# Optimization experiments

Hardware: AMD Instinct MI355X
Metric: run time of the kernel (lower is better)

## Reference

```python
import jax, jax.numpy as jnp
import numpy as np
import math

HEAD_DIM = 64
N_NEWTON_ITER = 6


def _top_k_sum_selection(T, select_number, mask):
    # T: [B,H,N,D]; mask: [B,N] int (True/1 => masked out for selection, per source)
    B, H, N, D = T.shape
    big = jnp.finfo(T.dtype).max
    # select_type == 'sum' -> non-absolute row sums over feature dim, excluding token 0
    somme = jnp.sum(T[:, :, 1:, :], axis=-1)                      # [B,H,N-1]
    somme = jnp.where(mask[:, None, 1:].astype(bool), -big, somme)
    top = jax.lax.top_k(somme, select_number - 1)[1] + 1          # [B,H,M-1]
    top = jnp.concatenate(
        [top, jnp.zeros((B, H, 1), dtype=top.dtype)], axis=-1)    # always keep token 0
    index = jnp.sort(top, axis=-1)                                 # [B,H,M]
    nt = jnp.take_along_axis(T, index[..., None], axis=2)          # [B,H,M,D]
    return nt, index


def _m_matrix_composition(C, r_index):
    # C: [B,H,N,M]; r_index: [B,H,M] -> gather selected rows -> [B,H,M,M]
    return jnp.take_along_axis(C, r_index[..., None], axis=2)


def _iterative_inv(mat, n_iter=N_NEWTON_ITER):
    M = mat.shape[-1]
    I = jnp.eye(M, dtype=mat.dtype)
    Km = mat
    # init_option == 'original': global max of column sums
    V = (1.0 / jnp.max(jnp.sum(Km, axis=-2))) * jnp.swapaxes(Km, -1, -2)
    for _ in range(n_iter):
        KV = jnp.matmul(Km, V)
        V = jnp.matmul(0.25 * V,
                       13.0 * I - jnp.matmul(KV, 15.0 * I - jnp.matmul(KV, 7.0 * I - KV)))
    return V


def setup_inputs() -> dict:
    key = jax.random.key(0)
    k1, k2, k3, k4 = jax.random.split(key, 4)
    B, H, N, D = 4, 8, 4096, 64
    return {
        "Q": jax.random.normal(k1, (B, H, N, D), dtype=jnp.float32),
        "K": jax.random.normal(k2, (B, H, N, D), dtype=jnp.float32),
        "V": jax.random.normal(k3, (B, H, N, D), dtype=jnp.float32),
        "mask": jax.random.randint(k4, (B, N), 0, 2, dtype=jnp.int32),
        "select_number": 64,
    }


def reference(Q, K, V, mask, select_number):
    big = jnp.finfo(Q.dtype).max
    Qs = Q / math.sqrt(HEAD_DIM)
    nc, _ = _top_k_sum_selection(K, select_number, mask)           # [B,H,M,D]
    nr, r_index = _top_k_sum_selection(Qs, select_number, mask)    # [B,H,M,D]
    c = jnp.einsum('bhnd,bhmd->bhnm', Qs, nc)                      # [B,H,N,M]
    r = jnp.einsum('bhmd,bhnd->bhmn', nr, K)                       # [B,H,M,N]
    # forward path fills where ~mask (mask==0 => masked)
    r = jnp.where(mask[:, None, None, :].astype(bool), r, -big)
    kernel_1 = jax.nn.softmax(c, axis=-1)                          # [B,H,N,M]
    u = _m_matrix_composition(kernel_1, r_index)                   # [B,H,M,M]
    kernel_3 = jax.nn.softmax(r, axis=-1)                          # [B,H,M,N]
    kernel_2_inv = _iterative_inv(u)                               # [B,H,M,M]
    X = jnp.matmul(kernel_1, jnp.matmul(kernel_2_inv, jnp.matmul(kernel_3, V)))
    return X
```

## Files before the change

### kernel.cpp

```cpp
#include <hip/hip_runtime.h>
#include <float.h>

#define BB 4
#define HH 8
#define BHN 32
#define NTOK 4096
#define DD 64
#define MM 64
#define PAD 68
#define GPART 16

typedef _Float16 f16;
typedef __attribute__((ext_vector_type(4))) _Float16 f16x4;
typedef __attribute__((ext_vector_type(8))) _Float16 f16x8;
typedef __attribute__((ext_vector_type(4))) float f32x4;

union V8U { f16x8 v; f16x4 q[2]; };

__device__ __forceinline__ void fsplit(float v, f16* h, f16* l) {
  f16 hh = (f16)v;
  *h = hh;
  *l = (f16)(v - (float)hh);
}

__device__ __forceinline__ f32x4 mm2(f16x8 a0, f16x8 a1, f16x8 b0, f16x8 b1) {
  f32x4 c = {0.f, 0.f, 0.f, 0.f};
  c = __builtin_amdgcn_mfma_f32_16x16x32_f16(a0, b0, c, 0, 0, 0);
  c = __builtin_amdgcn_mfma_f32_16x16x32_f16(a1, b1, c, 0, 0, 0);
  return c;
}

__device__ __forceinline__ f32x4 mm6(f16x8 ah0, f16x8 ah1, f16x8 al0, f16x8 al1,
                                     f16x8 bh0, f16x8 bh1, f16x8 bl0, f16x8 bl1) {
  f32x4 a = {0.f, 0.f, 0.f, 0.f};
  f32x4 b = {0.f, 0.f, 0.f, 0.f};
  a = __builtin_amdgcn_mfma_f32_16x16x32_f16(ah0, bh0, a, 0, 0, 0);
  a = __builtin_amdgcn_mfma_f32_16x16x32_f16(ah0, bl0, a, 0, 0, 0);
  a = __builtin_amdgcn_mfma_f32_16x16x32_f16(al0, bh0, a, 0, 0, 0);
  b = __builtin_amdgcn_mfma_f32_16x16x32_f16(ah1, bh1, b, 0, 0, 0);
  b = __builtin_amdgcn_mfma_f32_16x16x32_f16(ah1, bl1, b, 0, 0, 0);
  b = __builtin_amdgcn_mfma_f32_16x16x32_f16(al1, bh1, b, 0, 0, 0);
  return a + b;
}

template<int LDA, int LDB>
__device__ __forceinline__ void mm_acc(float acc[4][4],
    const float (*A)[LDA], const float (*B)[LDB], int ti, int tj) {
  #pragma unroll
  for (int k4 = 0; k4 < 16; ++k4) {
    float a[4][4], b[4][4];
    #pragma unroll
    for (int x = 0; x < 4; ++x) {
      float4 t = *(const float4*)&A[ti*4+x][k4*4];
      a[x][0]=t.x; a[x][1]=t.y; a[x][2]=t.z; a[x][3]=t.w;
    }
    #pragma unroll
    for (int kk = 0; kk < 4; ++kk) {
      float4 t = *(const float4*)&B[k4*4+kk][tj*4];
      b[kk][0]=t.x; b[kk][1]=t.y; b[kk][2]=t.z; b[kk][3]=t.w;
    }
    #pragma unroll
    for (int kk = 0; kk < 4; ++kk)
      #pragma unroll
      for (int x = 0; x < 4; ++x)
        #pragma unroll
        for (int y = 0; y < 4; ++y)
          acc[x][y] = fmaf(a[x][kk], b[kk][y], acc[x][y]);
  }
}

__global__ __launch_bounds__(256) void k_somme(const float* __restrict__ Kg,
    const float* __restrict__ Qg, const int* __restrict__ mask,
    float* __restrict__ somK, float* __restrict__ somQ) {
  int tid = threadIdx.x;
  int lane = tid & 63;
  long grow = (long)blockIdx.x * 16 + (tid >> 6) * 4 + (lane >> 4);
  int which = grow >= (long)(BHN * NTOK);
  long row = which ? grow - (long)BHN * NTOK : grow;
  int n = (int)(row & (NTOK - 1));
  int bh = (int)(row >> 12);
  int b = bh >> 3;
  const float* src = which ? Qg : Kg;
  float4 v = *((const float4*)(src + row * DD) + (lane & 15));
  float s = v.x + v.y + v.z + v.w;
  s += __shfl_xor(s, 1); s += __shfl_xor(s, 2);
  s += __shfl_xor(s, 4); s += __shfl_xor(s, 8);
  if ((lane & 15) == 0) {
    float out = (n == 0 || mask[b * NTOK + n] != 0) ? -FLT_MAX : s;
    (which ? somQ : somK)[row] = out;
  }
}

__global__ __launch_bounds__(256) void k_select(const float* __restrict__ Kg,
    const float* __restrict__ Qg, const float* __restrict__ somK,
    const float* __restrict__ somQ, float* __restrict__ nc, float* __restrict__ nr) {
  int bh = blockIdx.x;
  int which = blockIdx.y;
  __shared__ unsigned int keys[NTOK];
  __shared__ unsigned int wb[4][256];
  __shared__ int wsum[4];
  __shared__ int wsumB[4];
  __shared__ int sh_bin, sh_need;
  __shared__ int sel[MM];
  int tid = threadIdx.x, wave = tid >> 6, lane = tid & 63;
  const float* som = (which ? somQ : somK) + (long)bh * NTOK;
  for (int i = tid; i < NTOK; i += 256) {
    float f = som[i];
    unsigned int u = __float_as_uint(f);
    u = (u & 0x80000000u) ? ~u : (u | 0x80000000u);
    keys[i] = (i == 0) ? 0u : u;
  }
  unsigned int pref = 0; int need = MM - 1;
  for (int pass = 0; pass < 4; ++pass) {
    int shift = 24 - pass * 8;
    unsigned int pm = (pass == 0) ? 0u : (0xFFFFFFFFu << (32 - 8 * pass));
    unsigned int* wbf = (unsigned int*)wb;
    wbf[tid] = 0; wbf[tid + 256] = 0; wbf[tid + 512] = 0; wbf[tid + 768] = 0;
    __syncthreads();
    for (int i = tid; i < NTOK; i += 256) {
      unsigned int k = keys[i];
      if ((k & pm) == pref) atomicAdd(&wb[wave][(k >> shift) & 255], 1u);
    }
    __syncthreads();
    int binr = 255 - tid;
    int cnt = (int)(wb[0][binr] + wb[1][binr] + wb[2][binr] + wb[3][binr]);
    int v = cnt;
    #pragma unroll
    for (int d = 1; d < 64; d <<= 1) {
      int t = __shfl_up(v, d);
      if (lane >= d) v += t;
    }
    if (lane == 63) wsum[wave] = v;
    __syncthreads();
    int off = 0;
    #pragma unroll
    for (int w = 0; w < 4; ++w) off += (w < wave) ? wsum[w] : 0;
    v += off;
    int above = v - cnt;
    if (v >= need && above < need) { sh_bin = binr; sh_need = need - above; }
    __syncthreads();
    pref |= ((unsigned int)sh_bin) << shift;
    need = sh_need;
  }
  unsigned int thr = pref;

  int base = tid * 16;
  int ctie = 0;
  #pragma unroll
  for (int j = 0; j < 16; ++j) ctie += (keys[base + j] == thr);
  int v2 = ctie;
  #pragma unroll
  for (int d = 1; d < 64; d <<= 1) {
    int t = __shfl_up(v2, d);
    if (lane >= d) v2 += t;
  }
  if (lane == 63) wsum[wave] = v2;
  __syncthreads();
  int offt = 0;
  #pragma unroll
  for (int w = 0; w < 4; ++w) offt += (w < wave) ? wsum[w] : 0;
  int tie_excl = v2 + offt - ctie;

  int tieoff = tie_excl, cnt2 = 0;
  #pragma unroll
  for (int j = 0; j < 16; ++j) {
    unsigned int k = keys[base + j];
    int f = (k > thr) ? 1 : 0;
    if (k == thr) { f = (tieoff < need) ? 1 : 0; ++tieoff; }
    if (base + j == 0) f = 1;
    cnt2 += f;
  }
  int v3 = cnt2;
  #pragma unroll
  for (int d = 1; d < 64; d <<= 1) {
    int t = __shfl_up(v3, d);
    if (lane >= d) v3 += t;
  }
  if (lane == 63) wsumB[wave] = v3;
  __syncthreads();
  int offc = 0;
  #pragma unroll
  for (int w = 0; w < 4; ++w) offc += (w < wave) ? wsumB[w] : 0;
  int o = v3 + offc - cnt2;
  tieoff = tie_excl;
  #pragma unroll
  for (int j = 0; j < 16; ++j) {
    unsigned int k = keys[base + j];
    int f = (k > thr) ? 1 : 0;
    if (k == thr) { f = (tieoff < need) ? 1 : 0; ++tieoff; }
    if (base + j == 0) f = 1;
    if (f) sel[o++] = base + j;
  }
  __syncthreads();

  const float* src = which ? Qg : Kg;
  float* dst = (which ? nr : nc) + (long)bh * MM * DD;
  float scale = which ? 0.125f : 1.0f;
  for (int e = tid; e < MM * 16; e += 256) {
    int i = e >> 4, d4 = e & 15;
    float4 v = *(const float4*)&src[((long)bh * NTOK + sel[i]) * DD + d4 * 4];
    v.x *= scale; v.y *= scale; v.z *= scale; v.w *= scale;
    *(float4*)&dst[i * DD + d4 * 4] = v;
  }
}

__global__ __launch_bounds__(256) void k_u(const float* __restrict__ nc,
    const float* __restrict__ nr, float* __restrict__ u, float* __restrict__ smax) {
  int bh = blockIdx.x, tid = threadIdx.x, ti = tid >> 4, tj = tid & 15;
  __shared__ float A[MM][PAD];
  __shared__ float BT[DD][MM];
  __shared__ float cs[4][MM];
  for (int e = tid; e < 1024; e += 256) {
    int m = e >> 4, d4 = e & 15;
    *(float4*)&A[m][d4*4] = *(const float4*)&nr[(long)bh*MM*DD + m*DD + d4*4];
    float4 c = *(const float4*)&nc[(long)bh*MM*DD + m*DD + d4*4];
    BT[d4*4+0][m] = c.x; BT[d4*4+1][m] = c.y; BT[d4*4+2][m] = c.z; BT[d4*4+3][m] = c.w;
  }
  __syncthreads();
  float acc[4][4] = {};
  mm_acc<PAD, MM>(acc, A, BT, ti, tj);
  float e_[4][4];
  #pragma unroll
  for (int x = 0; x < 4; ++x)
    #pragma unroll
    for (int y = 0; y < 4; ++y) e_[x][y] = expf(acc[x][y]);
  float rsx[4];
  #pragma unroll
  for (int x = 0; x < 4; ++x) {
    rsx[x] = e_[x][0] + e_[x][1] + e_[x][2] + e_[x][3];
    rsx[x] += __shfl_xor(rsx[x], 1); rsx[x] += __shfl_xor(rsx[x], 2);
    rsx[x] += __shfl_xor(rsx[x], 4); rsx[x] += __shfl_xor(rsx[x], 8);
  }
  float cp[4] = {0.f, 0.f, 0.f, 0.f};
  #pragma unroll
  for (int x = 0; x < 4; ++x) {
    float inv = 1.f / rsx[x];
    float v0 = e_[x][0]*inv, v1 = e_[x][1]*inv, v2 = e_[x][2]*inv, v3 = e_[x][3]*inv;
    cp[0] += v0; cp[1] += v1; cp[2] += v2; cp[3] += v3;
    float4 o; o.x = v0; o.y = v1; o.z = v2; o.w = v3;
    *(float4*)&u[(long)bh*MM*MM + (ti*4+x)*MM + tj*4] = o;
  }
  #pragma unroll
  for (int y = 0; y < 4; ++y) {
    cp[y] += __shfl_xor(cp[y], 16);
    cp[y] += __shfl_xor(cp[y], 32);
  }
  if (((tid >> 4) & 3) == 0) {
    #pragma unroll
    for (int y = 0; y < 4; ++y) cs[tid >> 6][tj*4 + y] = cp[y];
  }
  __syncthreads();
  if (tid < 64) {
    float tot = cs[0][tid] + cs[1][tid] + cs[2][tid] + cs[3][tid];
    for (int off = 32; off; off >>= 1) tot = fmaxf(tot, __shfl_xor(tot, off));
    if (tid == 0) smax[bh] = tot;
  }
}

__device__ void newton_dev(char* smem, const float* __restrict__ u,
    const float* __restrict__ smax, float* __restrict__ vinv, int bh) {
  f16 (*VT_h)[72] = (f16(*)[72])(smem);
  f16 (*VT_l)[72] = (f16(*)[72])(smem + 9216);
  f16 (*Vr_h)[72] = (f16(*)[72])(smem + 18432);
  f16 (*Vr_l)[72] = (f16(*)[72])(smem + 27648);
  f16 (*PT_h)[72] = (f16(*)[72])(smem + 36864);
  f16 (*PT_l)[72] = (f16(*)[72])(smem + 46080);
  f16 (*RT_h)[72] = (f16(*)[72])(smem + 55296);
  f16 (*RT_l)[72] = (f16(*)[72])(smem + 64512);
  int tid = threadIdx.x;
  int wave = tid >> 6, lane = tid & 63;
  int wr = wave >> 1, wc = wave & 1;
  int lm = lane & 15, hi = lane >> 4;

  float gmx = smax[0];
  #pragma unroll
  for (int i = 1; i < 32; ++i) gmx = fmaxf(gmx, smax[i]);
  float c0 = 1.0f / gmx;

  const float* pu = u + (long)bh * MM * MM;
  for (int e = tid; e < 4096; e += 512) {
    int i = e >> 6, j = e & 63;
    float sv = pu[e] * c0;
    f16 h, l;
    fsplit(sv, &h, &l);
    VT_h[i][j] = h; VT_l[i][j] = l;
    Vr_h[j][i] = h; Vr_l[j][i] = l;
  }
  f16x8 kb_h[2], kb_l[2];
  {
    const float* p = pu + (wr*16 + lm) * 64;
    float kv[16];
    *(float4*)&kv[0]  = *(const float4*)(p + hi*8);
    *(float4*)&kv[4]  = *(const float4*)(p + hi*8 + 4);
    *(float4*)&kv[8]  = *(const float4*)(p + 32 + hi*8);
    *(float4*)&kv[12] = *(const float4*)(p + 36 + hi*8);
    #pragma unroll
    for (int j = 0; j < 8; ++j) {
      f16 h, l;
      fsplit(kv[j], &h, &l);     kb_h[0][j] = h; kb_l[0][j] = l;
      fsplit(kv[8+j], &h, &l);   kb_h[1][j] = h; kb_l[1][j] = l;
    }
  }
  __syncthreads();

  for (int it = 0; it < 6; ++it) {
    const bool PR = (it >= 3);
    const bool last = (it == 5);

    f32x4 st[4];
    #pragma unroll
    for (int g = 0; g < 4; ++g) {
      f16x8 ah0 = *(const f16x8*)&VT_h[g*16 + lm][hi*8];
      f16x8 ah1 = *(const f16x8*)&VT_h[g*16 + lm][32 + hi*8];
      if (PR) {
        f16x8 al0 = *(const f16x8*)&VT_l[g*16 + lm][hi*8];
        f16x8 al1 = *(const f16x8*)&VT_l[g*16 + lm][32 + hi*8];
        st[g] = mm6(ah0, ah1, al0, al1, kb_h[0], kb_h[1], kb_l[0], kb_l[1]);
      } else {
        st[g] = mm2(ah0, ah1, kb_h[0], kb_h[1]);
      }
    }
    f16x8 sa_h[2], sa_l[2];
    #pragma unroll
    for (int g = 0; g < 4; ++g)
      #pragma unroll
      for (int r = 0; r < 4; ++r) {
        if (PR) {
          f16 h, l; fsplit(st[g][r], &h, &l);
          sa_h[g >> 1][(g & 1)*4 + r] = h;
          sa_l[g >> 1][(g & 1)*4 + r] = l;
        } else {
          sa_h[g >> 1][(g & 1)*4 + r] = (f16)st[g][r];
        }
      }
    #pragma unroll
    for (int g = 0; g < 4; ++g) {
      if ((g >> 1) == wc) {
        #pragma unroll
        for (int r = 0; r < 4; ++r) {
          int i = g*16 + hi*4 + r, j = wr*16 + lm;
          float pv = (i == j ? 7.f : 0.f) - st[g][r];
          if (PR) {
            f16 h, l; fsplit(pv, &h, &l);
            PT_h[i][j] = h; PT_l[i][j] = l;
          } else {
            PT_h[i][j] = (f16)pv;
          }
        }
      }
    }
    __syncthreads();

    #pragma unroll
    for (int cc2 = 0; cc2 < 2; ++cc2) {
      int cc = wc*2 + cc2;
      V8U bh0, bh1, bl0, bl1;
      bh0.q[0] = *(const f16x4*)&PT_h[cc*16 + lm][hi*4];
      bh0.q[1] = *(const f16x4*)&PT_h[cc*16 + lm][16 + hi*4];
      bh1.q[0] = *(const f16x4*)&PT_h[cc*16 + lm][32 + hi*4];
      bh1.q[1] = *(const f16x4*)&PT_h[cc*16 + lm][48 + hi*4];
      f32x4 a;
      if (PR) {
        bl0.q[0] = *(const f16x4*)&PT_l[cc*16 + lm][hi*4];
        bl0.q[1] = *(const f16x4*)&PT_l[cc*16 + lm][16 + hi*4];
        bl1.q[0] = *(const f16x4*)&PT_l[cc*16 + lm][32 + hi*4];
        bl1.q[1] = *(const f16x4*)&PT_l[cc*16 + lm][48 + hi*4];
        a = mm6(sa_h[0], sa_h[1], sa_l[0], sa_l[1], bh0.v, bh1.v, bl0.v, bl1.v);
      } else {
        a = mm2(sa_h[0], sa_h[1], bh0.v, bh1.v);
      }
      f16x4 wh, wl;
      #pragma unroll
      for (int r = 0; r < 4; ++r) {
        int row = wr*16 + hi*4 + r, col = cc*16 + lm;
        float rv = (row == col ? 15.f : 0.f) - a[r];
        if (PR) { f16 h, l; fsplit(rv, &h, &l); wh[r] = h; wl[r] = l; }
        else wh[r] = (f16)rv;
      }
      *(f16x4*)&RT_h[cc*16 + lm][wr*16 + hi*4] = wh;
      if (PR) *(f16x4*)&RT_l[cc*16 + lm][wr*16 + hi*4] = wl;
    }
    __syncthreads();

    #pragma unroll
    for (int cc2 = 0; cc2 < 2; ++cc2) {
      int cc = wc*2 + cc2;
      V8U bh0, bh1, bl0, bl1;
      bh0.q[0] = *(const f16x4*)&RT_h[cc*16 + lm][hi*4];
      bh0.q[1] = *(const f16x4*)&RT_h[cc*16 + lm][16 + hi*4];
      bh1.q[0] = *(const f16x4*)&RT_h[cc*16 + lm][32 + hi*4];
      bh1.q[1] = *(const f16x4*)&RT_h[cc*16 + lm][48 + hi*4];
      f32x4 a;
      if (PR) {
        bl0.q[0] = *(const f16x4*)&RT_l[cc*16 + lm][hi*4];
        bl0.q[1] = *(const f16x4*)&RT_l[cc*16 + lm][16 + hi*4];
        bl1.q[0] = *(const f16x4*)&RT_l[cc*16 + lm][32 + hi*4];
        bl1.q[1] = *(const f16x4*)&RT_l[cc*16 + lm][48 + hi*4];
        a = mm6(sa_h[0], sa_h[1], sa_l[0], sa_l[1], bh0.v, bh1.v, bl0.v, bl1.v);
      } else {
        a = mm2(sa_h[0], sa_h[1], bh0.v, bh1.v);
      }
      f16x4 wh, wl;
      #pragma unroll
      for (int r = 0; r < 4; ++r) {
        int row = wr*16 + hi*4 + r, col = cc*16 + lm;
        float wv = (row == col ? 13.f : 0.f) - a[r];
        if (PR) { f16 h, l; fsplit(wv, &h, &l); wh[r] = h; wl[r] = l; }
        else wh[r] = (f16)wv;
      }
      *(f16x4*)&PT_h[cc*16 + lm][wr*16 + hi*4] = wh;
      if (PR) *(f16x4*)&PT_l[cc*16 + lm][wr*16 + hi*4] = wl;
    }
    __syncthreads();

    f16x8 vh0 = *(const f16x8*)&Vr_h[wr*16 + lm][hi*8];
    f16x8 vh1 = *(const f16x8*)&Vr_h[wr*16 + lm][32 + hi*8];
    f16x8 vl0, vl1;
    if (PR) {
      vl0 = *(const f16x8*)&Vr_l[wr*16 + lm][hi*8];
      vl1 = *(const f16x8*)&Vr_l[wr*16 + lm][32 + hi*8];
    }
    #pragma unroll
    for (int cc2 = 0; cc2 < 2; ++cc2) {
      int cc = wc*2 + cc2;
      f16x8 wh0 = *(const f16x8*)&PT_h[cc*16 + lm][hi*8];
      f16x8 wh1 = *(const f16x8*)&PT_h[cc*16 + lm][32 + hi*8];
      f32x4 a;
      if (PR) {
        f16x8 wl0 = *(const f16x8*)&PT_l[cc*16 + lm][hi*8];
        f16x8 wl1 = *(const f16x8*)&PT_l[cc*16 + lm][32 + hi*8];
        a = mm6(vh0, vh1, vl0, vl1, wh0, wh1, wl0, wl1);
      } else {
        a = mm2(vh0, vh1, wh0, wh1);
      }
      if (last) {
        #pragma unroll
        for (int r = 0; r < 4; ++r)
          vinv[(long)bh*MM*MM + (wr*16 + hi*4 + r)*MM + cc*16 + lm] = 0.25f * a[r];
      } else {
        f16x4 th, tl;
        #pragma unroll
        for (int r = 0; r < 4; ++r) {
          float vv = 0.25f * a[r];
          f16 h, l; fsplit(vv, &h, &l);
          Vr_h[wr*16 + hi*4 + r][cc*16 + lm] = h;
          Vr_l[wr*16 + hi*4 + r][cc*16 + lm] = l;
          th[r] = h; tl[r] = l;
        }
        *(f16x4*)&VT_h[cc*16 + lm][wr*16 + hi*4] = th;
        *(f16x4*)&VT_l[cc*16 + lm][wr*16 + hi*4] = tl;
      }
    }
    __syncthreads();
  }
}

__device__ void w3_dev(char* smem, const float* __restrict__ Kg,
    const float* __restrict__ Vg, const int* __restrict__ maskg,
    const float* __restrict__ nr, float* __restrict__ nump,
    float* __restrict__ denp, int idx) {
  int bh = idx >> 3, grp = idx & 7, b = bh >> 3;
  int tid = threadIdx.x;
  int half = tid >> 8, t = tid & 255;
  f16 (*Ks)[72] = (f16(*)[72])(smem + half * 18432);
  f16 (*Vs)[72] = (f16(*)[72])(smem + half * 18432 + 9216);
  float* kmul = (float*)(smem + 36864) + half * 64;
  int lane = tid & 63;
  int lm = lane & 15, hi = lane >> 4;
  int wv = t >> 6;
  int m0 = wv * 16;
  int gslot = grp * 2 + half;

  f16x8 nrf[2];
  {
    const float* p = nr + (long)bh*MM*DD + (long)(m0 + lm)*DD + hi*8;
    float4 q0 = *(const float4*)p;
    float4 q1 = *(const float4*)(p + 4);
    float4 q2 = *(const float4*)(p + 32);
    float4 q3 = *(const float4*)(p + 36);
    nrf[0][0]=(f16)q0.x; nrf[0][1]=(f16)q0.y; nrf[0][2]=(f16)q0.z; nrf[0][3]=(f16)q0.w;
    nrf[0][4]=(f16)q1.x; nrf[0][5]=(f16)q1.y; nrf[0][6]=(f16)q1.z; nrf[0][7]=(f16)q1.w;
    nrf[1][0]=(f16)q2.x; nrf[1][1]=(f16)q2.y; nrf[1][2]=(f16)q2.z; nrf[1][3]=(f16)q2.w;
    nrf[1][4]=(f16)q3.x; nrf[1][5]=(f16)q3.y; nrf[1][6]=(f16)q3.z; nrf[1][7]=(f16)q3.w;
  }

  f32x4 nacc[4];
  #pragma unroll
  for (int dt = 0; dt < 4; ++dt) nacc[dt] = (f32x4){0.f, 0.f, 0.f, 0.f};
  float dsum = 0.f;

  for (int sc = 0; sc < 4; ++sc) {
    int n0c = (gslot * 4 + sc) * 64;
    if (sc) __syncthreads();
    for (int s = t; s < 1024; s += 256) {
      int row = s >> 4, c4 = s & 15;
      float4 kv = *(const float4*)&Kg[((long)bh*NTOK + n0c + row)*DD + c4*4];
      float4 vv = *(const float4*)&Vg[((long)bh*NTOK + n0c + row)*DD + c4*4];
      f16x4 kk = {(f16)kv.x, (f16)kv.y, (f16)kv.z, (f16)kv.w};
      f16x4 vv4 = {(f16)vv.x, (f16)vv.y, (f16)vv.z, (f16)vv.w};
      *(f16x4*)&Ks[row][c4*4] = kk;
      *(f16x4*)&Vs[row][c4*4] = vv4;
    }
    if (t < 64) kmul[t] = maskg[b * NTOK + n0c + t] ? 1.f : 0.f;
    __syncthreads();

    f32x4 stv[4];
    #pragma unroll
    for (int g = 0; g < 4; ++g) {
      f16x8 a0 = *(const f16x8*)&Ks[g*16 + lm][hi*8];
      f16x8 a1 = *(const f16x8*)&Ks[g*16 + lm][32 + hi*8];
      stv[g] = mm2(a0, a1, nrf[0], nrf[1]);
    }
    f16x8 pa[2];
    #pragma unroll
    for (int g = 0; g < 4; ++g) {
      #pragma unroll
      for (int r = 0; r < 4; ++r) {
        float p = __expf(stv[g][r]) * kmul[g*16 + hi*4 + r];
        dsum += p;
        pa[g >> 1][(g & 1)*4 + r] = (f16)p;
      }
    }
    #pragma unroll
    for (int dt = 0; dt < 4; ++dt) {
      f16x8 vb0, vb1;
      #pragma unroll
      for (int j = 0; j < 8; ++j) {
        int nrow = hi*4 + (j & 3) + 16*(j >> 2);
        vb0[j] = Vs[nrow][dt*16 + lm];
        vb1[j] = Vs[32 + nrow][dt*16 + lm];
      }
      nacc[dt] = __builtin_amdgcn_mfma_f32_16x16x32_f16(pa[0], vb0, nacc[dt], 0, 0, 0);
      nacc[dt] = __builtin_amdgcn_mfma_f32_16x16x32_f16(pa[1], vb1, nacc[dt], 0, 0, 0);
    }
  }
  float* pnum = nump + ((long)bh * GPART + gslot) * (MM * DD);
  #pragma unroll
  for (int dt = 0; dt < 4; ++dt)
    #pragma unroll
    for (int r = 0; r < 4; ++r)
      pnum[(m0 + hi*4 + r)*DD + dt*16 + lm] = nacc[dt][r];
  float d2 = dsum + __shfl_xor(dsum, 16);
  d2 += __shfl_xor(d2, 32);
  if (lane < 16)
    denp[((long)bh * GPART + gslot) * MM + m0 + lane] = d2;
}

__global__ __launch_bounds__(512) void k_mix(const float* __restrict__ u,
    const float* __restrict__ smax, float* __restrict__ vinv,
    const float* __restrict__ Kg, const float* __restrict__ Vg,
    const int* __restrict__ maskg, const float* __restrict__ nr,
    float* __restrict__ nump, float* __restrict__ denp) {
  __shared__ __align__(16) char smem[73728];
  if (blockIdx.x < 32)
    newton_dev(smem, u, smax, vinv, blockIdx.x);
  else
    w3_dev(smem, Kg, Vg, maskg, nr, nump, denp, blockIdx.x - 32);
}

__global__ __launch_bounds__(256) void k_z(const float* __restrict__ vinv,
    const float* __restrict__ nump, const float* __restrict__ denp, float* __restrict__ Zg) {
  int bh = blockIdx.x, tid = threadIdx.x, ti = tid >> 4, tj = tid & 15;
  __shared__ float A[MM][PAD];
  __shared__ float W[MM][MM];
  __shared__ float dn[MM];
  if (tid < 64) {
    float s = 0.f;
    #pragma unroll
    for (int g = 0; g < GPART; ++g) s += denp[((long)bh * GPART + g) * MM + tid];
    dn[tid] = s;
  }
  for (int e = tid; e < 1024; e += 256) {
    int m = e >> 4, d4 = e & 15;
    *(float4*)&A[m][d4*4] = *(const float4*)&vinv[(long)bh*MM*MM + m*MM + d4*4];
  }
  __syncthreads();
  for (int e = tid; e < 1024; e += 256) {
    int m = e >> 4, d4 = e & 15;
    float4 s = {0.f, 0.f, 0.f, 0.f};
    #pragma unroll
    for (int g = 0; g < GPART; ++g) {
      float4 t = *(const float4*)&nump[((long)bh * GPART + g) * (MM*DD) + m*DD + d4*4];
      s.x += t.x; s.y += t.y; s.z += t.z; s.w += t.w;
    }
    float inv = 1.f / dn[m];
    s.x *= inv; s.y *= inv; s.z *= inv; s.w *= inv;
    *(float4*)&W[m][d4*4] = s;
  }
  __syncthreads();
  float acc[4][4] = {};
  mm_acc<PAD, MM>(acc, A, W, ti, tj);
  #pragma unroll
  for (int x = 0; x < 4; ++x) {
    float4 o; o.x = acc[x][0]; o.y = acc[x][1]; o.z = acc[x][2]; o.w = acc[x][3];
    *(float4*)&Zg[(long)bh*MM*DD + (ti*4+x)*DD + tj*4] = o;
  }
}

__global__ __launch_bounds__(256) void k_final(const float* __restrict__ Qg,
    const float* __restrict__ nc, const float* __restrict__ Zg, float* __restrict__ Xg) {
  int bh = blockIdx.x, chunk = blockIdx.y;
  int tid = threadIdx.x;
  int wave = tid >> 6, lane = tid & 63;
  int lm = lane & 15, hi = lane >> 4;
  int n0 = chunk * 64;
  __shared__ f16 Qs[64][72];
  __shared__ f16 Ncs[64][72];
  __shared__ f16 Zs[64][72];
  for (int s = tid; s < 1024; s += 256) {
    int row = s >> 4, c4 = s & 15;
    float4 q = *(const float4*)&Qg[((long)bh*NTOK + n0 + row)*DD + c4*4];
    f16x4 qq = {(f16)(q.x*0.125f), (f16)(q.y*0.125f), (f16)(q.z*0.125f), (f16)(q.w*0.125f)};
    *(f16x4*)&Qs[row][c4*4] = qq;
    float4 cv = *(const float4*)&nc[(long)bh*MM*DD + row*DD + c4*4];
    f16x4 cc = {(f16)cv.x, (f16)cv.y, (f16)cv.z, (f16)cv.w};
    *(f16x4*)&Ncs[row][c4*4] = cc;
    float4 zv = *(const float4*)&Zg[(long)bh*MM*DD + row*DD + c4*4];
    f16x4 zz = {(f16)zv.x, (f16)zv.y, (f16)zv.z, (f16)zv.w};
    *(f16x4*)&Zs[row][c4*4] = zz;
  }
  __syncthreads();

  f16x8 qb0 = *(const f16x8*)&Qs[wave*16 + lm][hi*8];
  f16x8 qb1 = *(const f16x8*)&Qs[wave*16 + lm][32 + hi*8];
  f32x4 stv[4];
  #pragma unroll
  for (int mt = 0; mt < 4; ++mt) {
    f16x8 a0 = *(const f16x8*)&Ncs[mt*16 + lm][hi*8];
    f16x8 a1 = *(const f16x8*)&Ncs[mt*16 + lm][32 + hi*8];
    stv[mt] = mm2(a0, a1, qb0, qb1);
  }
  f16x8 pa[2];
  float dsum = 0.f;
  #pragma unroll
  for (int mt = 0; mt < 4; ++mt) {
    #pragma unroll
    for (int r = 0; r < 4; ++r) {
      float p = __expf(stv[mt][r]);
      dsum += p;
      pa[mt >> 1][(mt & 1)*4 + r] = (f16)p;
    }
  }
  float dtot = dsum + __shfl_xor(dsum, 16);
  dtot += __shfl_xor(dtot, 32);
  f32x4 xacc[4];
  #pragma unroll
  for (int dt = 0; dt < 4; ++dt) {
    f16x8 zb0, zb1;
    #pragma unroll
    for (int j = 0; j < 8; ++j) {
      int mrow = hi*4 + (j & 3) + 16*(j >> 2);
      zb0[j] = Zs[mrow][dt*16 + lm];
      zb1[j] = Zs[32 + mrow][dt*16 + lm];
    }
    f32x4 c = {0.f, 0.f, 0.f, 0.f};
    c = __builtin_amdgcn_mfma_f32_16x16x32_f16(pa[0], zb0, c, 0, 0, 0);
    c = __builtin_amdgcn_mfma_f32_16x16x32_f16(pa[1], zb1, c, 0, 0, 0);
    xacc[dt] = c;
  }
  float rn[4];
  #pragma unroll
  for (int r = 0; r < 4; ++r) rn[r] = 1.f / __shfl(dtot, hi*4 + r);
  #pragma unroll
  for (int dt = 0; dt < 4; ++dt)
    #pragma unroll
    for (int r = 0; r < 4; ++r)
      Xg[((long)bh*NTOK + n0 + wave*16 + hi*4 + r)*DD + dt*16 + lm] = xacc[dt][r] * rn[r];
}

extern "C" void kernel_launch(void* const* d_in, const int* in_sizes, int n_in,
                              void* d_out, int out_size, void* d_ws, size_t ws_size,
                              hipStream_t stream) {
  (void)in_sizes; (void)n_in; (void)out_size; (void)ws_size;
  const float* Qp = (const float*)d_in[0];
  const float* Kp = (const float*)d_in[1];
  const float* Vp = (const float*)d_in[2];
  const int* maskp = (const int*)d_in[3];
  float* out = (float*)d_out;

  float* wsf = (float*)d_ws;
  float* NUMP = wsf;
  float* DENP = NUMP + (long)BHN * GPART * MM * DD;
  float* SMAX = DENP + BHN * GPART * MM;
  float* NC = SMAX + 32;
  float* NR = NC + BHN * MM * DD;
  float* U  = NR + BHN * MM * DD;
  float* VI = U  + BHN * MM * MM;
  float* Zb = VI + BHN * MM * MM;
  float* SK = Zb + BHN * MM * DD;
  float* SQ = SK + BHN * NTOK;

  k_somme<<<16384, 256, 0, stream>>>(Kp, Qp, maskp, SK, SQ);
  k_select<<<dim3(32, 2), 256, 0, stream>>>(Kp, Qp, SK, SQ, NC, NR);
  k_u<<<32, 256, 0, stream>>>(NC, NR, U, SMAX);
  k_mix<<<32 + 256, 512, 0, stream>>>(U, SMAX, VI, Kp, Vp, maskp, NR, NUMP, DENP);
  k_z<<<32, 256, 0, stream>>>(VI, NUMP, DENP, Zb);
  k_final<<<dim3(32, 64), 256, 0, stream>>>(Qp, NC, Zb, out);
}
```

Measured before the change: 82.03 us.

## Restructure Newton inverse into two-wave teams with register-resident operands

The Newton-Schulz inverse now uses a team of two waves per matrix, with four matrices per block, instead of one 512-thread block per matrix. Each wave keeps its K and V column operands in registers and chains the three inner products through registers. Only S and V go through shared memory, stored as packed hi/lo f16 pairs, which cuts barriers per iteration from four to two. The mixed kernel's shared memory grows to 136 KB, which may lower occupancy for the co-scheduled w3 blocks. Register pressure also rises, since each wave holds many fragment arrays.

New measurement: 146.6 us. +78.7%, slower.

```diff
diff --git a/kernel.cpp b/kernel.cpp
--- a/kernel.cpp
+++ b/kernel.cpp
@@ -14,13 +14,19 @@
 typedef __attribute__((ext_vector_type(4))) _Float16 f16x4;
 typedef __attribute__((ext_vector_type(8))) _Float16 f16x8;
 typedef __attribute__((ext_vector_type(4))) float f32x4;
-
-union V8U { f16x8 v; f16x4 q[2]; };
+typedef __attribute__((ext_vector_type(4))) unsigned int u32x4;
 
 __device__ __forceinline__ void fsplit(float v, f16* h, f16* l) {
   f16 hh = (f16)v;
   *h = hh;
   *l = (f16)(v - (float)hh);
+}
+
+__device__ __forceinline__ unsigned int pck(f16 h, f16 l) {
+  union { unsigned int x; f16 f[2]; } t; t.f[0] = h; t.f[1] = l; return t.x;
+}
+__device__ __forceinline__ void unp(unsigned int u, f16* h, f16* l) {
+  union { unsigned int x; f16 f[2]; } t; t.x = u; *h = t.f[0]; *l = t.f[1];
 }
 
 __device__ __forceinline__ f32x4 mm2(f16x8 a0, f16x8 a1, f16x8 b0, f16x8 b1) {
@@ -257,201 +263,215 @@
   }
 }
 
-__device__ void newton_dev(char* smem, const float* __restrict__ u,
-    const float* __restrict__ smax, float* __restrict__ vinv, int bh) {
-  f16 (*VT_h)[72] = (f16(*)[72])(smem);
-  f16 (*VT_l)[72] = (f16(*)[72])(smem + 9216);
-  f16 (*Vr_h)[72] = (f16(*)[72])(smem + 18432);
-  f16 (*Vr_l)[72] = (f16(*)[72])(smem + 27648);
-  f16 (*PT_h)[72] = (f16(*)[72])(smem + 36864);
-  f16 (*PT_l)[72] = (f16(*)[72])(smem + 46080);
-  f16 (*RT_h)[72] = (f16(*)[72])(smem + 55296);
-  f16 (*RT_l)[72] = (f16(*)[72])(smem + 64512);
-  int tid = threadIdx.x;
-  int wave = tid >> 6, lane = tid & 63;
-  int wr = wave >> 1, wc = wave & 1;
+__device__ void newton2(unsigned int* __restrict__ STp, unsigned int* __restrict__ VrTp,
+    const float* __restrict__ pu, float c0, float* __restrict__ vout,
+    int side, int lane) {
+  const int RS = 68;
   int lm = lane & 15, hi = lane >> 4;
 
-  float gmx = smax[0];
-  #pragma unroll
-  for (int i = 1; i < 32; ++i) gmx = fmaxf(gmx, smax[i]);
-  float c0 = 1.0f / gmx;
-
-  const float* pu = u + (long)bh * MM * MM;
-  for (int e = tid; e < 4096; e += 512) {
-    int i = e >> 6, j = e & 63;
-    float sv = pu[e] * c0;
-    f16 h, l;
-    fsplit(sv, &h, &l);
-    VT_h[i][j] = h; VT_l[i][j] = l;
-    Vr_h[j][i] = h; Vr_l[j][i] = l;
-  }
-  f16x8 kb_h[2], kb_l[2];
+  f16x8 kbh[4][2], kbl[4][2];
+  f16x8 vbh[2][2], vbl[2][2];
   {
-    const float* p = pu + (wr*16 + lm) * 64;
-    float kv[16];
-    *(float4*)&kv[0]  = *(const float4*)(p + hi*8);
-    *(float4*)&kv[4]  = *(const float4*)(p + hi*8 + 4);
-    *(float4*)&kv[8]  = *(const float4*)(p + 32 + hi*8);
-    *(float4*)&kv[12] = *(const float4*)(p + 36 + hi*8);
-    #pragma unroll
-    for (int j = 0; j < 8; ++j) {
-      f16 h, l;
-      fsplit(kv[j], &h, &l);     kb_h[0][j] = h; kb_l[0][j] = l;
-      fsplit(kv[8+j], &h, &l);   kb_h[1][j] = h; kb_l[1][j] = l;
-    }
-  }
-  __syncthreads();
-
+    float kv[4][16];
+    #pragma unroll
+    for (int I = 0; I < 4; ++I) {
+      const float* pr = pu + (16*I + lm) * 64;
+      #pragma unroll
+      for (int m = 0; m < 2; ++m)
+        #pragma unroll
+        for (int s = 0; s < 2; ++s) {
+          float4 q = *(const float4*)(pr + 32*m + 16*s + 4*hi);
+          kv[I][m*8+s*4+0] = q.x; kv[I][m*8+s*4+1] = q.y;
+          kv[I][m*8+s*4+2] = q.z; kv[I][m*8+s*4+3] = q.w;
+        }
+    }
+    #pragma unroll
+    for (int I = 0; I < 4; ++I)
+      #pragma unroll
+      for (int m = 0; m < 2; ++m)
+        #pragma unroll
+        for (int j = 0; j < 8; ++j) {
+          f16 h, l; fsplit(kv[I][m*8+j], &h, &l);
+          kbh[I][m][j] = h; kbl[I][m][j] = l;
+        }
+    #pragma unroll
+    for (int jj = 0; jj < 2; ++jj)
+      #pragma unroll
+      for (int m = 0; m < 2; ++m)
+        #pragma unroll
+        for (int j = 0; j < 8; ++j) {
+          float v0 = side ? kv[2+jj][m*8+j] : kv[jj][m*8+j];
+          f16 h, l; fsplit(c0 * v0, &h, &l);
+          vbh[jj][m][j] = h; vbl[jj][m][j] = l;
+        }
+    if (!side) {
+      #pragma unroll
+      for (int I = 0; I < 4; ++I)
+        #pragma unroll
+        for (int m = 0; m < 2; ++m)
+          #pragma unroll
+          for (int s = 0; s < 2; ++s)
+            #pragma unroll
+            for (int r = 0; r < 4; ++r) {
+              f16 h, l; fsplit(c0 * kv[I][m*8+s*4+r], &h, &l);
+              VrTp[(32*m+16*s+4*hi+r)*RS + 16*I + lm] = pck(h, l);
+            }
+    }
+  }
+
+  #pragma unroll 1
   for (int it = 0; it < 6; ++it) {
     const bool PR = (it >= 3);
     const bool last = (it == 5);
 
-    f32x4 st[4];
-    #pragma unroll
-    for (int g = 0; g < 4; ++g) {
-      f16x8 ah0 = *(const f16x8*)&VT_h[g*16 + lm][hi*8];
-      f16x8 ah1 = *(const f16x8*)&VT_h[g*16 + lm][32 + hi*8];
-      if (PR) {
-        f16x8 al0 = *(const f16x8*)&VT_l[g*16 + lm][hi*8];
-        f16x8 al1 = *(const f16x8*)&VT_l[g*16 + lm][32 + hi*8];
-        st[g] = mm6(ah0, ah1, al0, al1, kb_h[0], kb_h[1], kb_l[0], kb_l[1]);
-      } else {
-        st[g] = mm2(ah0, ah1, kb_h[0], kb_h[1]);
-      }
-    }
-    f16x8 sa_h[2], sa_l[2];
-    #pragma unroll
-    for (int g = 0; g < 4; ++g)
-      #pragma unroll
-      for (int r = 0; r < 4; ++r) {
-        if (PR) {
-          f16 h, l; fsplit(st[g][r], &h, &l);
-          sa_h[g >> 1][(g & 1)*4 + r] = h;
-          sa_l[g >> 1][(g & 1)*4 + r] = l;
-        } else {
-          sa_h[g >> 1][(g & 1)*4 + r] = (f16)st[g][r];
+    f32x4 c1[4][2];
+    #pragma unroll
+    for (int I = 0; I < 4; ++I)
+      #pragma unroll
+      for (int jj = 0; jj < 2; ++jj)
+        c1[I][jj] = PR ? mm6(kbh[I][0], kbh[I][1], kbl[I][0], kbl[I][1],
+                             vbh[jj][0], vbh[jj][1], vbl[jj][0], vbl[jj][1])
+                       : mm2(kbh[I][0], kbh[I][1], vbh[jj][0], vbh[jj][1]);
+    f16x8 pbh[2][2], pbl[2][2];
+    #pragma unroll
+    for (int jj = 0; jj < 2; ++jj) {
+      int cJ = 32*side + 16*jj + lm;
+      #pragma unroll
+      for (int m = 0; m < 2; ++m)
+        #pragma unroll
+        for (int s = 0; s < 2; ++s)
+          #pragma unroll
+          for (int r = 0; r < 4; ++r) {
+            int k = 32*m + 16*s + 4*hi + r;
+            float pv = ((k == cJ) ? 7.f : 0.f) - c1[2*m+s][jj][r];
+            if (PR) { f16 h, l; fsplit(pv, &h, &l); pbh[jj][m][s*4+r] = h; pbl[jj][m][s*4+r] = l; }
+            else pbh[jj][m][s*4+r] = (f16)pv;
+          }
+    }
+    #pragma unroll
+    for (int I = 0; I < 4; ++I)
+      #pragma unroll
+      for (int jj = 0; jj < 2; ++jj)
+        #pragma unroll
+        for (int r = 0; r < 4; ++r) {
+          float sval = c1[I][jj][r];
+          f16 h, l;
+          if (PR) fsplit(sval, &h, &l); else { h = (f16)sval; l = (f16)0.f; }
+          STp[(16*I + 4*hi + r)*RS + 32*side + 16*jj + lm] = pck(h, l);
+        }
+    __syncthreads();
+
+    f16x8 sah[4][2], sal[4][2];
+    #pragma unroll
+    for (int I = 0; I < 4; ++I)
+      #pragma unroll
+      for (int m = 0; m < 2; ++m) {
+        u32x4 a = *(const u32x4*)&STp[(16*I + lm)*RS + 32*m + 4*hi];
+        u32x4 b = *(const u32x4*)&STp[(16*I + lm)*RS + 32*m + 16 + 4*hi];
+        #pragma unroll
+        for (int r = 0; r < 4; ++r) {
+          f16 h, l;
+          unp(a[r], &h, &l); sah[I][m][r] = h;   sal[I][m][r] = l;
+          unp(b[r], &h, &l); sah[I][m][4+r] = h; sal[I][m][4+r] = l;
         }
       }
-    #pragma unroll
-    for (int g = 0; g < 4; ++g) {
-      if ((g >> 1) == wc) {
+
+    f32x4 c2[4][2];
+    #pragma unroll
+    for (int I = 0; I < 4; ++I)
+      #pragma unroll
+      for (int jj = 0; jj < 2; ++jj)
+        c2[I][jj] = PR ? mm6(sah[I][0], sah[I][1], sal[I][0], sal[I][1],
+                             pbh[jj][0], pbh[jj][1], pbl[jj][0], pbl[jj][1])
+                       : mm2(sah[I][0], sah[I][1], pbh[jj][0], pbh[jj][1]);
+    f16x8 rbh[2][2], rbl[2][2];
+    #pragma unroll
+    for (int jj = 0; jj < 2; ++jj) {
+      int cJ = 32*side + 16*jj + lm;
+      #pragma unroll
+      for (int m = 0; m < 2; ++m)
+        #pragma unroll
+        for (int s = 0; s < 2; ++s)
+          #pragma unroll
+          for (int r = 0; r < 4; ++r) {
+            int k = 32*m + 16*s + 4*hi + r;
+            float rv = ((k == cJ) ? 15.f : 0.f) - c2[2*m+s][jj][r];
+            if (PR) { f16 h, l; fsplit(rv, &h, &l); rbh[jj][m][s*4+r] = h; rbl[jj][m][s*4+r] = l; }
+            else rbh[jj][m][s*4+r] = (f16)rv;
+          }
+    }
+
+    f32x4 c3[4][2];
+    #pragma unroll
+    for (int I = 0; I < 4; ++I)
+      #pragma unroll
+      for (int jj = 0; jj < 2; ++jj)
+        c3[I][jj] = PR ? mm6(sah[I][0], sah[I][1], sal[I][0], sal[I][1],
+                             rbh[jj][0], rbh[jj][1], rbl[jj][0], rbl[jj][1])
+                       : mm2(sah[I][0], sah[I][1], rbh[jj][0], rbh[jj][1]);
+    f16x8 wbh[2][2], wbl[2][2];
+    #pragma unroll
+    for (int jj = 0; jj < 2; ++jj) {
+      int cJ = 32*side + 16*jj + lm;
+      #pragma unroll
+      for (int m = 0; m < 2; ++m)
+        #pragma unroll
+        for (int s = 0; s < 2; ++s)
+          #pragma unroll
+          for (int r = 0; r < 4; ++r) {
+            int k = 32*m + 16*s + 4*hi + r;
+            float wv = ((k == cJ) ? 13.f : 0.f) - c3[2*m+s][jj][r];
+            if (PR) { f16 h, l; fsplit(wv, &h, &l); wbh[jj][m][s*4+r] = h; wbl[jj][m][s*4+r] = l; }
+            else wbh[jj][m][s*4+r] = (f16)wv;
+          }
+    }
+
+    f16x8 vah[4][2], val_[4][2];
+    #pragma unroll
+    for (int I = 0; I < 4; ++I)
+      #pragma unroll
+      for (int m = 0; m < 2; ++m) {
+        u32x4 a = *(const u32x4*)&VrTp[(16*I + lm)*RS + 32*m + 4*hi];
+        u32x4 b = *(const u32x4*)&VrTp[(16*I + lm)*RS + 32*m + 16 + 4*hi];
         #pragma unroll
         for (int r = 0; r < 4; ++r) {
-          int i = g*16 + hi*4 + r, j = wr*16 + lm;
-          float pv = (i == j ? 7.f : 0.f) - st[g][r];
-          if (PR) {
-            f16 h, l; fsplit(pv, &h, &l);
-            PT_h[i][j] = h; PT_l[i][j] = l;
-          } else {
-            PT_h[i][j] = (f16)pv;
-          }
+          f16 h, l;
+          unp(a[r], &h, &l); vah[I][m][r] = h;   val_[I][m][r] = l;
+          unp(b[r], &h, &l); vah[I][m][4+r] = h; val_[I][m][4+r] = l;
         }
       }
-    }
     __syncthreads();
 
-    #pragma unroll
-    for (int cc2 = 0; cc2 < 2; ++cc2) {
-      int cc = wc*2 + cc2;
-      V8U bh0, bh1, bl0, bl1;
-      bh0.q[0] = *(const f16x4*)&PT_h[cc*16 + lm][hi*4];
-      bh0.q[1] = *(const f16x4*)&PT_h[cc*16 + lm][16 + hi*4];
-      bh1.q[0] = *(const f16x4*)&PT_h[cc*16 + lm][32 + hi*4];
-      bh1.q[1] = *(const f16x4*)&PT_h[cc*16 + lm][48 + hi*4];
-      f32x4 a;
-      if (PR) {
-        bl0.q[0] = *(const f16x4*)&PT_l[cc*16 + lm][hi*4];
-        bl0.q[1] = *(const f16x4*)&PT_l[cc*16 + lm][16 + hi*4];
-        bl1.q[0] = *(const f16x4*)&PT_l[cc*16 + lm][32 + hi*4];
-        bl1.q[1] = *(const f16x4*)&PT_l[cc*16 + lm][48 + hi*4];
-        a = mm6(sa_h[0], sa_h[1], sa_l[0], sa_l[1], bh0.v, bh1.v, bl0.v, bl1.v);
-      } else {
-        a = mm2(sa_h[0], sa_h[1], bh0.v, bh1.v);
-      }
-      f16x4 wh, wl;
-      #pragma unroll
-      for (int r = 0; r < 4; ++r) {
-        int row = wr*16 + hi*4 + r, col = cc*16 + lm;
-        float rv = (row == col ? 15.f : 0.f) - a[r];
-        if (PR) { f16 h, l; fsplit(rv, &h, &l); wh[r] = h; wl[r] = l; }
-        else wh[r] = (f16)rv;
-      }
-      *(f16x4*)&RT_h[cc*16 + lm][wr*16 + hi*4] = wh;
-      if (PR) *(f16x4*)&RT_l[cc*16 + lm][wr*16 + hi*4] = wl;
-    }
-    __syncthreads();
-
-    #pragma unroll
-    for (int cc2 = 0; cc2 < 2; ++cc2) {
-      int cc = wc*2 + cc2;
-      V8U bh0, bh1, bl0, bl1;
-      bh0.q[0] = *(const f16x4*)&RT_h[cc*16 + lm][hi*4];
-      bh0.q[1] = *(const f16x4*)&RT_h[cc*16 + lm][16 + hi*4];
-      bh1.q[0] = *(const f16x4*)&RT_h[cc*16 + lm][32 + hi*4];
-      bh1.q[1] = *(const f16x4*)&RT_h[cc*16 + lm][48 + hi*4];
-      f32x4 a;
-      if (PR) {
-        bl0.q[0] = *(const f16x4*)&RT_l[cc*16 + lm][hi*4];
-        bl0.q[1] = *(const f16x4*)&RT_l[cc*16 + lm][16 + hi*4];
-        bl1.q[0] = *(const f16x4*)&RT_l[cc*16 + lm][32 + hi*4];
-        bl1.q[1] = *(const f16x4*)&RT_l[cc*16 + lm][48 + hi*4];
-        a = mm6(sa_h[0], sa_h[1], sa_l[0], sa_l[1], bh0.v, bh1.v, bl0.v, bl1.v);
-      } else {
-        a = mm2(sa_h[0], sa_h[1], bh0.v, bh1.v);
-      }
-      f16x4 wh, wl;
-      #pragma unroll
-      for (int r = 0; r < 4; ++r) {
-        int row = wr*16 + hi*4 + r, col = cc*16 + lm;
-        float wv = (row == col ? 13.f : 0.f) - a[r];
-        if (PR) { f16 h, l; fsplit(wv, &h, &l); wh[r] = h; wl[r] = l; }
-        else wh[r] = (f16)wv;
-      }
-      *(f16x4*)&PT_h[cc*16 + lm][wr*16 + hi*4] = wh;
-      if (PR) *(f16x4*)&PT_l[cc*16 + lm][wr*16 + hi*4] = wl;
-    }
-    __syncthreads();
-
-    f16x8 vh0 = *(const f16x8*)&Vr_h[wr*16 + lm][hi*8];
-    f16x8 vh1 = *(const f16x8*)&Vr_h[wr*16 + lm][32 + hi*8];
-    f16x8 vl0, vl1;
-    if (PR) {
-      vl0 = *(const f16x8*)&Vr_l[wr*16 + lm][hi*8];
-      vl1 = *(const f16x8*)&Vr_l[wr*16 + lm][32 + hi*8];
-    }
-    #pragma unroll
-    for (int cc2 = 0; cc2 < 2; ++cc2) {
-      int cc = wc*2 + cc2;
-      f16x8 wh0 = *(const f16x8*)&PT_h[cc*16 + lm][hi*8];
-      f16x8 wh1 = *(const f16x8*)&PT_h[cc*16 + lm][32 + hi*8];
-      f32x4 a;
-      if (PR) {
-        f16x8 wl0 = *(const f16x8*)&PT_l[cc*16 + lm][hi*8];
-        f16x8 wl1 = *(const f16x8*)&PT_l[cc*16 + lm][32 + hi*8];
-        a = mm6(vh0, vh1, vl0, vl1, wh0, wh1, wl0, wl1);
-      } else {
-        a = mm2(vh0, vh1, wh0, wh1);
-      }
-      if (last) {
-        #pragma unroll
-        for (int r = 0; r < 4; ++r)
-          vinv[(long)bh*MM*MM + (wr*16 + hi*4 + r)*MM + cc*16 + lm] = 0.25f * a[r];
-      } else {
-        f16x4 th, tl;
-        #pragma unroll
-        for (int r = 0; r < 4; ++r) {
-          float vv = 0.25f * a[r];
-          f16 h, l; fsplit(vv, &h, &l);
-          Vr_h[wr*16 + hi*4 + r][cc*16 + lm] = h;
-          Vr_l[wr*16 + hi*4 + r][cc*16 + lm] = l;
-          th[r] = h; tl[r] = l;
-        }
-        *(f16x4*)&VT_h[cc*16 + lm][wr*16 + hi*4] = th;
-        *(f16x4*)&VT_l[cc*16 + lm][wr*16 + hi*4] = tl;
-      }
-    }
-    __syncthreads();
+    f32x4 c4[4][2];
+    #pragma unroll
+    for (int I = 0; I < 4; ++I)
+      #pragma unroll
+      for (int jj = 0; jj < 2; ++jj)
+        c4[I][jj] = PR ? mm6(vah[I][0], vah[I][1], val_[I][0], val_[I][1],
+                             wbh[jj][0], wbh[jj][1], wbl[jj][0], wbl[jj][1])
+                       : mm2(vah[I][0], vah[I][1], wbh[jj][0], wbh[jj][1]);
+    if (last) {
+      #pragma unroll
+      for (int I = 0; I < 4; ++I)
+        #pragma unroll
+        for (int jj = 0; jj < 2; ++jj)
+          #pragma unroll
+          for (int r = 0; r < 4; ++r)
+            vout[(16*I + 4*hi + r)*MM + 32*side + 16*jj + lm] = 0.25f * c4[I][jj][r];
+    } else {
+      #pragma unroll
+      for (int I = 0; I < 4; ++I)
+        #pragma unroll
+        for (int jj = 0; jj < 2; ++jj)
+          #pragma unroll
+          for (int r = 0; r < 4; ++r) {
+            float vv = 0.25f * c4[I][jj][r];
+            f16 h, l; fsplit(vv, &h, &l);
+            vbh[jj][I>>1][(I&1)*4 + r] = h;
+            vbl[jj][I>>1][(I&1)*4 + r] = l;
+            VrTp[(16*I + 4*hi + r)*RS + 32*side + 16*jj + lm] = pck(h, l);
+          }
+    }
   }
 }
 
@@ -551,11 +571,22 @@
     const float* __restrict__ Kg, const float* __restrict__ Vg,
     const int* __restrict__ maskg, const float* __restrict__ nr,
     float* __restrict__ nump, float* __restrict__ denp) {
-  __shared__ __align__(16) char smem[73728];
-  if (blockIdx.x < 32)
-    newton_dev(smem, u, smax, vinv, blockIdx.x);
-  else
-    w3_dev(smem, Kg, Vg, maskg, nr, nump, denp, blockIdx.x - 32);
+  __shared__ __align__(16) char smem[139264];
+  if (blockIdx.x < 8) {
+    int tid = threadIdx.x;
+    int wave = tid >> 6, lane = tid & 63;
+    int team = wave >> 1, side = wave & 1;
+    int bh = blockIdx.x * 4 + team;
+    unsigned int* STp = (unsigned int*)smem + team * 8704;
+    unsigned int* VrTp = STp + 4352;
+    float gmx = smax[0];
+    #pragma unroll
+    for (int i = 1; i < 32; ++i) gmx = fmaxf(gmx, smax[i]);
+    newton2(STp, VrTp, u + (long)bh * MM * MM, 1.0f / gmx,
+            vinv + (long)bh * MM * MM, side, lane);
+  } else {
+    w3_dev(smem, Kg, Vg, maskg, nr, nump, denp, blockIdx.x - 8);
+  }
 }
 
 __global__ __launch_bounds__(256) void k_z(const float* __restrict__ vinv,
@@ -693,7 +724,7 @@
   k_somme<<<16384, 256, 0, stream>>>(Kp, Qp, maskp, SK, SQ);
   k_select<<<dim3(32, 2), 256, 0, stream>>>(Kp, Qp, SK, SQ, NC, NR);
   k_u<<<32, 256, 0, stream>>>(NC, NR, U, SMAX);
-  k_mix<<<32 + 256, 512, 0, stream>>>(U, SMAX, VI, Kp, Vp, maskp, NR, NUMP, DENP);
+  k_mix<<<8 + 256, 512, 0, stream>>>(U, SMAX, VI, Kp, Vp, maskp, NR, NUMP, DENP);
   k_z<<<32, 256, 0, stream>>>(VI, NUMP, DENP, Zb);
   k_final<<<dim3(32, 64), 256, 0, stream>>>(Qp, NC, Zb, out);
 }
```
